# Optimization experiments

Measured on AMD Instinct MI355X. Metric: run time of the kernel, lower is better.

## Reference

```python
import jax, jax.numpy as jnp
import numpy as np

NUM_ENT = 50000
NUM_REL = 500
DIM = 128
BATCH = 32
INIT_RHO = -5.0


def setup_inputs() -> dict:
    key = jax.random.key(0)
    k1, k2, k3 = jax.random.split(key, 3)
    ent_center = jax.random.uniform(k1, (NUM_ENT, 2 * DIM), minval=-0.1, maxval=0.1, dtype=jnp.float32)
    ent_rho = jnp.full((NUM_ENT, DIM), INIT_RHO, dtype=jnp.float32)
    rel_center = jax.random.uniform(k2, (NUM_REL, DIM), minval=-np.pi, maxval=np.pi, dtype=jnp.float32)
    rel_rho = jnp.full((NUM_REL, DIM), INIT_RHO, dtype=jnp.float32)
    pos_triplets = jax.random.randint(k3, (BATCH, 3), 0, NUM_REL, dtype=jnp.int64)
    return {
        "ent_center": ent_center,
        "ent_rho": ent_rho,
        "rel_center": rel_center,
        "rel_rho": rel_rho,
        "pos_triplets": pos_triplets,
    }


def reference(ent_center, ent_rho, rel_center, rel_rho, pos_triplets):
    # All-entity embeddings: center split into (re, im) halves, radius via softplus.
    u_re, u_im = jnp.split(ent_center, 2, axis=-1)          # [N, D] each
    u_r = jax.nn.softplus(ent_rho)                           # [N, D]

    h_idx = pos_triplets[:, 0]
    r_idx = pos_triplets[:, 1]

    hc = ent_center[h_idx]                                   # [B, 2D]
    hr = jax.nn.softplus(ent_rho[h_idx])                     # [B, D]
    rc_phase = rel_center[r_idx]                             # [B, D]
    rr = jax.nn.softplus(rel_rho[r_idx])                     # [B, D]

    hc_re, hc_im = jnp.split(hc, 2, axis=-1)                 # [B, D]
    cos_r = jnp.cos(rc_phase)
    sin_r = jnp.sin(rc_phase)
    pred_re = hc_re * cos_r - hc_im * sin_r                  # [B, D]
    pred_im = hc_re * sin_r + hc_im * cos_r                  # [B, D]
    pred_r = hr + rr                                         # [B, D]

    # Broadcast L2 (complex magnitude) distance to every entity: [B, N]
    diff_re = pred_re[:, None, :] - u_re[None, :, :]         # [B, N, D]
    diff_im = pred_im[:, None, :] - u_im[None, :, :]         # [B, N, D]
    dist_c = jnp.sqrt(diff_re ** 2 + diff_im ** 2).sum(axis=-1)  # [B, N]

    # sum over dim of (pred_r + u_r) broadcast == sum(pred_r) + sum(u_r)
    sum_r = pred_r.sum(axis=-1)[:, None] + u_r.sum(axis=-1)[None, :]  # [B, N]
    return sum_r - dist_c
```

## Files before the change

kernel.cpp:

```cpp
#include <hip/hip_runtime.h>
#include <math.h>

#define NENT 50000
#define NREL 500
#define DIMK 128
#define BATCH 32

#define WS_PRED 0
#define WS_PSUM 8192
#define WS_URSUM 8224

__device__ __forceinline__ float softplus_f(float x) {
    float e = __expf(-fabsf(x));
    return fmaxf(x, 0.0f) + __logf(1.0f + e);
}

__device__ __forceinline__ float fast_sqrtf(float x) {
#if __has_builtin(__builtin_amdgcn_sqrtf)
    return __builtin_amdgcn_sqrtf(x);
#else
    return sqrtf(x);
#endif
}

__device__ __forceinline__ int get_idx(const void* trip, int flat) {
    const long long* t64 = (const long long*)trip;
    const int* t32 = (const int*)trip;
    bool is64 = true;
    #pragma unroll 1
    for (int i = 0; i < 48; ++i) {
        long long v = t64[i];
        if (v < 0 || v >= NREL) { is64 = false; break; }
    }
    return is64 ? (int)t64[flat] : t32[flat];
}

__global__ __launch_bounds__(128)
void prep_kernel(const float* __restrict__ ent_center,
                 const float* __restrict__ ent_rho,
                 const float* __restrict__ rel_center,
                 const float* __restrict__ rel_rho,
                 const void* __restrict__ trip,
                 float* __restrict__ ws) {
    const int b = blockIdx.x;
    const int d = threadIdx.x;
    const int h = get_idx(trip, b * 3 + 0);
    const int r = get_idx(trip, b * 3 + 1);

    float hre = ent_center[h * 256 + d];
    float him = ent_center[h * 256 + 128 + d];
    float ph  = rel_center[r * 128 + d];
    float s = sinf(ph), c = cosf(ph);
    ws[WS_PRED + (b * 128 + d) * 2 + 0] = hre * c - him * s;
    ws[WS_PRED + (b * 128 + d) * 2 + 1] = hre * s + him * c;

    float pr = softplus_f(ent_rho[h * 128 + d]) + softplus_f(rel_rho[r * 128 + d]);
    #pragma unroll
    for (int off = 32; off > 0; off >>= 1) pr += __shfl_down(pr, off);
    __shared__ float tmp[2];
    if ((threadIdx.x & 63) == 0) tmp[threadIdx.x >> 6] = pr;
    __syncthreads();
    if (threadIdx.x == 0) ws[WS_PSUM + b] = tmp[0] + tmp[1];
}

__global__ __launch_bounds__(256)
void ursum_kernel(const float* __restrict__ ent_rho, float* __restrict__ ws) {
    const int wave = threadIdx.x >> 6, lane = threadIdx.x & 63;
    const int e = blockIdx.x * 4 + wave;
    if (e >= NENT) return;
    float2 v = *(const float2*)(ent_rho + (size_t)e * 128 + lane * 2);
    float s = softplus_f(v.x) + softplus_f(v.y);
    #pragma unroll
    for (int off = 32; off > 0; off >>= 1) s += __shfl_down(s, off);
    if (lane == 0) ws[WS_URSUM + e] = s;
}

__global__ __launch_bounds__(256, 3)
void score_kernel(const float* __restrict__ ent_center,
                  const float* __restrict__ ws,
                  float* __restrict__ out) {
    __shared__ float4 s_pred[2048];
    __shared__ float4 s_stage[1024];

    const int tid = threadIdx.x;
    const int wave = tid >> 6, lane = tid & 63;
    const int e0 = blockIdx.x * 64;
    const int q = tid & 7;
    const int et0 = tid >> 3;
    const float4* cen4 = (const float4*)ent_center;
    const float4* ws4 = (const float4*)ws;

    #pragma unroll
    for (int i = 0; i < 8; ++i) s_pred[tid + 256 * i] = ws4[tid + 256 * i];

    float4 g[4];
    auto GLOAD = [&](int c) {
        #pragma unroll
        for (int s = 0; s < 2; ++s)
            #pragma unroll
            for (int r = 0; r < 2; ++r) {
                int ge = e0 + et0 + 32 * r;
                if (ge > NENT - 1) ge = NENT - 1;
                g[s * 2 + r] = cen4[(size_t)ge * 64 + s * 32 + c * 8 + q];
            }
    };
    auto DSWRITE = [&]() {
        #pragma unroll
        for (int s = 0; s < 2; ++s)
            #pragma unroll
            for (int r = 0; r < 2; ++r) {
                int et = et0 + 32 * r;
                s_stage[(s * 8 + q) * 64 + (et ^ q)] = g[s * 2 + r];
            }
    };

    float acc[8];
    #pragma unroll
    for (int b = 0; b < 8; ++b) acc[b] = 0.0f;

    GLOAD(0);
    __syncthreads();
    #pragma unroll 1
    for (int c = 0; c < 4; ++c) {
        if (c) __syncthreads();
        DSWRITE();
        if (c < 3) GLOAD(c + 1);
        __syncthreads();
        #pragma unroll
        for (int dq = 0; dq < 8; ++dq) {
            const float4 ur = s_stage[dq * 64 + (lane ^ dq)];
            const float4 ui = s_stage[(8 + dq) * 64 + (lane ^ dq)];
            #pragma unroll
            for (int bb = 0; bb < 8; ++bb) {
                const int b = wave * 8 + bb;
                const int p0 = b * 64 + c * 16 + dq * 2;
                const float4 p01 = s_pred[p0];
                const float4 p23 = s_pred[p0 + 1];
                float dre, dmi, t;
                dre = p01.x - ur.x; dmi = p01.y - ui.x; t = dre * dre + dmi * dmi; acc[bb] += fast_sqrtf(t);
                dre = p01.z - ur.y; dmi = p01.w - ui.y; t = dre * dre + dmi * dmi; acc[bb] += fast_sqrtf(t);
                dre = p23.x - ur.z; dmi = p23.y - ui.z; t = dre * dre + dmi * dmi; acc[bb] += fast_sqrtf(t);
                dre = p23.z - ur.w; dmi = p23.w - ui.w; t = dre * dre + dmi * dmi; acc[bb] += fast_sqrtf(t);
            }
        }
    }

    const int e = e0 + lane;
    if (e < NENT) {
        const float ursum = ws[WS_URSUM + e];
        #pragma unroll
        for (int bb = 0; bb < 8; ++bb) {
            const int b = wave * 8 + bb;
            out[(size_t)b * NENT + e] = ws[WS_PSUM + b] + ursum - acc[bb];
        }
    }
}

extern "C" void kernel_launch(void* const* d_in, const int* in_sizes, int n_in,
                              void* d_out, int out_size, void* d_ws, size_t ws_size,
                              hipStream_t stream) {
    const float* ent_center = (const float*)d_in[0];
    const float* ent_rho    = (const float*)d_in[1];
    const float* rel_center = (const float*)d_in[2];
    const float* rel_rho    = (const float*)d_in[3];
    const void*  trip       = d_in[4];
    float* ws  = (float*)d_ws;
    float* out = (float*)d_out;

    ursum_kernel<<<(NENT + 3) / 4, 256, 0, stream>>>(ent_rho, ws);
    prep_kernel<<<BATCH, 128, 0, stream>>>(ent_center, ent_rho, rel_center, rel_rho, trip, ws);
    score_kernel<<<(NENT + 63) / 64, 256, 0, stream>>>(ent_center, ws, out);
}
```

Measured before the change: 160.1 us.

## Drop LDS pred staging, use wave-uniform scalar loads and 512-thread blocks

Result: slower. 168.3 us (+5.1%).

```diff
diff --git a/kernel.cpp b/kernel.cpp
--- a/kernel.cpp
+++ b/kernel.cpp
@@ -75,51 +75,38 @@
     if (lane == 0) ws[WS_URSUM + e] = s;
 }
 
-__global__ __launch_bounds__(256, 3)
+__global__ __launch_bounds__(512, 4)
 void score_kernel(const float* __restrict__ ent_center,
                   const float* __restrict__ ws,
                   float* __restrict__ out) {
-    __shared__ float4 s_pred[2048];
     __shared__ float4 s_stage[1024];
 
     const int tid = threadIdx.x;
-    const int wave = tid >> 6, lane = tid & 63;
+    const int lane = tid & 63;
+    const int wv = __builtin_amdgcn_readfirstlane(tid >> 6);
     const int e0 = blockIdx.x * 64;
     const int q = tid & 7;
-    const int et0 = tid >> 3;
+    const int et = tid >> 3;
     const float4* cen4 = (const float4*)ent_center;
-    const float4* ws4 = (const float4*)ws;
+    const float4* pred4 = (const float4*)(ws + WS_PRED);
 
-    #pragma unroll
-    for (int i = 0; i < 8; ++i) s_pred[tid + 256 * i] = ws4[tid + 256 * i];
-
-    float4 g[4];
+    float4 g[2];
     auto GLOAD = [&](int c) {
+        int ge = e0 + et;
+        if (ge > NENT - 1) ge = NENT - 1;
         #pragma unroll
         for (int s = 0; s < 2; ++s)
-            #pragma unroll
-            for (int r = 0; r < 2; ++r) {
-                int ge = e0 + et0 + 32 * r;
-                if (ge > NENT - 1) ge = NENT - 1;
-                g[s * 2 + r] = cen4[(size_t)ge * 64 + s * 32 + c * 8 + q];
-            }
+            g[s] = cen4[(size_t)ge * 64 + s * 32 + c * 8 + q];
     };
     auto DSWRITE = [&]() {
         #pragma unroll
         for (int s = 0; s < 2; ++s)
-            #pragma unroll
-            for (int r = 0; r < 2; ++r) {
-                int et = et0 + 32 * r;
-                s_stage[(s * 8 + q) * 64 + (et ^ q)] = g[s * 2 + r];
-            }
+            s_stage[(s * 8 + q) * 64 + (et ^ q)] = g[s];
     };
 
-    float acc[8];
-    #pragma unroll
-    for (int b = 0; b < 8; ++b) acc[b] = 0.0f;
+    float acc[4] = {0.0f, 0.0f, 0.0f, 0.0f};
 
     GLOAD(0);
-    __syncthreads();
     #pragma unroll 1
     for (int c = 0; c < 4; ++c) {
         if (c) __syncthreads();
@@ -130,17 +117,20 @@
         for (int dq = 0; dq < 8; ++dq) {
             const float4 ur = s_stage[dq * 64 + (lane ^ dq)];
             const float4 ui = s_stage[(8 + dq) * 64 + (lane ^ dq)];
+            float4 PA[4], PB[4];
             #pragma unroll
-            for (int bb = 0; bb < 8; ++bb) {
-                const int b = wave * 8 + bb;
-                const int p0 = b * 64 + c * 16 + dq * 2;
-                const float4 p01 = s_pred[p0];
-                const float4 p23 = s_pred[p0 + 1];
+            for (int bb = 0; bb < 4; ++bb) {
+                const int p0 = (wv * 4 + bb) * 64 + c * 16 + dq * 2;
+                PA[bb] = pred4[p0];
+                PB[bb] = pred4[p0 + 1];
+            }
+            #pragma unroll
+            for (int bb = 0; bb < 4; ++bb) {
                 float dre, dmi, t;
-                dre = p01.x - ur.x; dmi = p01.y - ui.x; t = dre * dre + dmi * dmi; acc[bb] += fast_sqrtf(t);
-                dre = p01.z - ur.y; dmi = p01.w - ui.y; t = dre * dre + dmi * dmi; acc[bb] += fast_sqrtf(t);
-                dre = p23.x - ur.z; dmi = p23.y - ui.z; t = dre * dre + dmi * dmi; acc[bb] += fast_sqrtf(t);
-                dre = p23.z - ur.w; dmi = p23.w - ui.w; t = dre * dre + dmi * dmi; acc[bb] += fast_sqrtf(t);
+                dre = PA[bb].x - ur.x; dmi = PA[bb].y - ui.x; t = dre * dre + dmi * dmi; acc[bb] += fast_sqrtf(t);
+                dre = PA[bb].z - ur.y; dmi = PA[bb].w - ui.y; t = dre * dre + dmi * dmi; acc[bb] += fast_sqrtf(t);
+                dre = PB[bb].x - ur.z; dmi = PB[bb].y - ui.z; t = dre * dre + dmi * dmi; acc[bb] += fast_sqrtf(t);
+                dre = PB[bb].z - ur.w; dmi = PB[bb].w - ui.w; t = dre * dre + dmi * dmi; acc[bb] += fast_sqrtf(t);
             }
         }
     }
@@ -149,8 +139,8 @@
     if (e < NENT) {
         const float ursum = ws[WS_URSUM + e];
         #pragma unroll
-        for (int bb = 0; bb < 8; ++bb) {
-            const int b = wave * 8 + bb;
+        for (int bb = 0; bb < 4; ++bb) {
+            const int b = wv * 4 + bb;
             out[(size_t)b * NENT + e] = ws[WS_PSUM + b] + ursum - acc[bb];
         }
     }
@@ -169,5 +159,5 @@
 
     ursum_kernel<<<(NENT + 3) / 4, 256, 0, stream>>>(ent_rho, ws);
     prep_kernel<<<BATCH, 128, 0, stream>>>(ent_center, ent_rho, rel_center, rel_rho, trip, ws);
-    score_kernel<<<(NENT + 63) / 64, 256, 0, stream>>>(ent_center, ws, out);
+    score_kernel<<<(NENT + 63) / 64, 512, 0, stream>>>(ent_center, ws, out);
 }
```

## Replace shared-memory pred tile with register-held values broadcast via readlane

Applied to the files above, without the earlier changes.

Result: slower. 169.4 us (+5.8%).

```diff
diff --git a/kernel.cpp b/kernel.cpp
--- a/kernel.cpp
+++ b/kernel.cpp
@@ -21,6 +21,10 @@
 #else
     return sqrtf(x);
 #endif
+}
+
+__device__ __forceinline__ float RL(float v, int l) {
+    return __uint_as_float(__builtin_amdgcn_readlane(__float_as_uint(v), l));
 }
 
 __device__ __forceinline__ int get_idx(const void* trip, int flat) {
@@ -75,23 +79,21 @@
     if (lane == 0) ws[WS_URSUM + e] = s;
 }
 
-__global__ __launch_bounds__(256, 3)
+__global__ __launch_bounds__(256, 4)
 void score_kernel(const float* __restrict__ ent_center,
                   const float* __restrict__ ws,
                   float* __restrict__ out) {
-    __shared__ float4 s_pred[2048];
     __shared__ float4 s_stage[1024];
 
     const int tid = threadIdx.x;
-    const int wave = tid >> 6, lane = tid & 63;
+    const int lane = tid & 63;
+    const int wv = tid >> 6;
     const int e0 = blockIdx.x * 64;
     const int q = tid & 7;
-    const int et0 = tid >> 3;
+    const int et = tid >> 3;
     const float4* cen4 = (const float4*)ent_center;
-    const float4* ws4 = (const float4*)ws;
 
-    #pragma unroll
-    for (int i = 0; i < 8; ++i) s_pred[tid + 256 * i] = ws4[tid + 256 * i];
+    const float* pbase = ws + WS_PRED + (size_t)(wv * 8 + (lane >> 3)) * 256 + (lane & 7);
 
     float4 g[4];
     auto GLOAD = [&](int c) {
@@ -99,7 +101,7 @@
         for (int s = 0; s < 2; ++s)
             #pragma unroll
             for (int r = 0; r < 2; ++r) {
-                int ge = e0 + et0 + 32 * r;
+                int ge = e0 + (et & 31) + 32 * r;
                 if (ge > NENT - 1) ge = NENT - 1;
                 g[s * 2 + r] = cen4[(size_t)ge * 64 + s * 32 + c * 8 + q];
             }
@@ -109,8 +111,8 @@
         for (int s = 0; s < 2; ++s)
             #pragma unroll
             for (int r = 0; r < 2; ++r) {
-                int et = et0 + 32 * r;
-                s_stage[(s * 8 + q) * 64 + (et ^ q)] = g[s * 2 + r];
+                int ee = (et & 31) + 32 * r;
+                s_stage[(s * 8 + q) * 64 + (ee ^ q)] = g[s * 2 + r];
             }
     };
 
@@ -119,28 +121,31 @@
     for (int b = 0; b < 8; ++b) acc[b] = 0.0f;
 
     GLOAD(0);
-    __syncthreads();
     #pragma unroll 1
     for (int c = 0; c < 4; ++c) {
         if (c) __syncthreads();
         DSWRITE();
         if (c < 3) GLOAD(c + 1);
+        float P[8];
+        #pragma unroll
+        for (int k = 0; k < 8; ++k) P[k] = pbase[c * 64 + k * 8];
         __syncthreads();
+
         #pragma unroll
         for (int dq = 0; dq < 8; ++dq) {
             const float4 ur = s_stage[dq * 64 + (lane ^ dq)];
             const float4 ui = s_stage[(8 + dq) * 64 + (lane ^ dq)];
             #pragma unroll
             for (int bb = 0; bb < 8; ++bb) {
-                const int b = wave * 8 + bb;
-                const int p0 = b * 64 + c * 16 + dq * 2;
-                const float4 p01 = s_pred[p0];
-                const float4 p23 = s_pred[p0 + 1];
                 float dre, dmi, t;
-                dre = p01.x - ur.x; dmi = p01.y - ui.x; t = dre * dre + dmi * dmi; acc[bb] += fast_sqrtf(t);
-                dre = p01.z - ur.y; dmi = p01.w - ui.y; t = dre * dre + dmi * dmi; acc[bb] += fast_sqrtf(t);
-                dre = p23.x - ur.z; dmi = p23.y - ui.z; t = dre * dre + dmi * dmi; acc[bb] += fast_sqrtf(t);
-                dre = p23.z - ur.w; dmi = p23.w - ui.w; t = dre * dre + dmi * dmi; acc[bb] += fast_sqrtf(t);
+                dre = RL(P[dq], bb * 8 + 0) - ur.x; dmi = RL(P[dq], bb * 8 + 1) - ui.x;
+                t = dre * dre + dmi * dmi; acc[bb] += fast_sqrtf(t);
+                dre = RL(P[dq], bb * 8 + 2) - ur.y; dmi = RL(P[dq], bb * 8 + 3) - ui.y;
+                t = dre * dre + dmi * dmi; acc[bb] += fast_sqrtf(t);
+                dre = RL(P[dq], bb * 8 + 4) - ur.z; dmi = RL(P[dq], bb * 8 + 5) - ui.z;
+                t = dre * dre + dmi * dmi; acc[bb] += fast_sqrtf(t);
+                dre = RL(P[dq], bb * 8 + 6) - ur.w; dmi = RL(P[dq], bb * 8 + 7) - ui.w;
+                t = dre * dre + dmi * dmi; acc[bb] += fast_sqrtf(t);
             }
         }
     }
@@ -150,7 +155,7 @@
         const float ursum = ws[WS_URSUM + e];
         #pragma unroll
         for (int bb = 0; bb < 8; ++bb) {
-            const int b = wave * 8 + bb;
+            const int b = wv * 8 + bb;
             out[(size_t)b * NENT + e] = ws[WS_PSUM + b] + ursum - acc[bb];
         }
     }
```
